# Performance work log

Hardware: AMD Instinct MI355X
Metric: run time of the kernel (lower is better)

Reference implementation:

```python
import jax, jax.numpy as jnp
import numpy as np

DEPTH, HEADS, DH, BUCKET, NHASH = 4, 8, 64, 64, 4
DIM, VOCAB, BATCH, SEQ = 512, 50000, 2, 2048
LN_EPS = 1e-5
SELF_ATTN_VAL = -5e4  # TOKEN_SELF_ATTN_VALUE in reformer_pytorch


def layer_norm(x, s, b):
    mu = x.mean(-1, keepdims=True)
    var = ((x - mu) ** 2).mean(-1, keepdims=True)
    return (x - mu) / jnp.sqrt(var + LN_EPS) * s + b


def sincos(t, dh):
    # FixedPositionalEmbedding: emb = cat(sin, cos) of t x dh/2 angles
    inv = 1.0 / (10000.0 ** (jnp.arange(0, dh, 2, dtype=jnp.float32) / dh))
    ang = jnp.arange(t, dtype=jnp.float32)[:, None] * inv[None, :]
    return jnp.sin(ang), jnp.cos(ang)


def apply_rotary(qk, sin, cos):
    # qk: [B*H, T, DH]; sin/cos: [T, DH/2]; interleaved-pair rotary as in reformer_pytorch
    sin2 = jnp.repeat(sin, 2, axis=-1)[None]
    cos2 = jnp.repeat(cos, 2, axis=-1)[None]
    xr = qk.reshape(qk.shape[0], qk.shape[1], -1, 2)
    rot = jnp.stack((-xr[..., 1], xr[..., 0]), axis=-1).reshape(qk.shape)
    return qk * cos2 + rot * sin2


def lsh_attention(qk, v, rot):
    # qk, v: [B, T, dh] (B = batch*heads, shared-QK); rot: [dh, NHASH, n_buckets//2]
    B, T, dh = qk.shape
    nb = T // BUCKET
    rv = jnp.einsum('btf,fhi->bhti', qk, rot)           # [B, NHASH, T, nb/2]
    rv = jnp.concatenate([rv, -rv], axis=-1)
    buckets = jnp.argmax(rv, axis=-1)                    # [B, NHASH, T]
    buckets = (buckets + (jnp.arange(NHASH) * nb)[None, :, None]).reshape(B, NHASH * T)
    ticker = jnp.arange(NHASH * T) % T
    key = T * buckets + ticker[None, :]                  # unique sort keys
    sticker = jnp.argsort(key, axis=-1)                  # [B, NHASH*T]
    undo = jnp.argsort(sticker, axis=-1)
    st = sticker % T
    sqk = jnp.take_along_axis(qk, st[:, :, None], axis=1)
    sv = jnp.take_along_axis(v, st[:, :, None], axis=1)
    C = NHASH * nb                                       # num chunks, each BUCKET long
    bq_t = st.reshape(B, C, BUCKET)
    bq = sqk.reshape(B, C, BUCKET, dh)
    bv = sv.reshape(B, C, BUCKET, dh)
    bk = bq / jnp.maximum(jnp.linalg.norm(bq, axis=-1, keepdims=True), 1e-12)

    def look_one_back(a):
        return jnp.concatenate([a, jnp.roll(a, 1, axis=1)], axis=2)

    bk, bv, bkv_t = look_one_back(bk), look_one_back(bv), look_one_back(bq_t)
    dots = jnp.einsum('bcie,bcje->bcij', bq, bk) * (dh ** -0.5)
    dots = jnp.where(bq_t[:, :, :, None] == bkv_t[:, :, None, :], SELF_ATTN_VAL, dots)
    lse = jax.nn.logsumexp(dots, axis=-1, keepdims=True)
    p = jnp.exp(dots - lse)
    bo = jnp.einsum('bcij,bcje->bcie', p, bv)
    so = bo.reshape(B, NHASH * T, dh)
    slog = lse.reshape(B, NHASH * T)
    o = jnp.take_along_axis(so, undo[:, :, None], axis=1).reshape(B, NHASH, T, dh)
    lg = jnp.take_along_axis(slog, undo, axis=1).reshape(B, NHASH, T, 1)
    w = jnp.exp(lg - jax.nn.logsumexp(lg, axis=1, keepdims=True))
    return jnp.sum(o * w, axis=1)                        # [B, T, dh]


def attn_block(x, s, bln, Wqk, Wv, Wo, bo, rot, sin, cos):
    b, t, _ = x.shape
    xn = layer_norm(x, s, bln)
    qk = (xn @ Wqk).reshape(b, t, HEADS, DH).transpose(0, 2, 1, 3).reshape(b * HEADS, t, DH)
    v = (xn @ Wv).reshape(b, t, HEADS, DH).transpose(0, 2, 1, 3).reshape(b * HEADS, t, DH)
    qk = apply_rotary(qk, sin, cos)
    o = lsh_attention(qk, v, rot)
    o = o.reshape(b, HEADS, t, DH).transpose(0, 2, 1, 3).reshape(b, t, HEADS * DH)
    return o @ Wo + bo


def ff_block(x, s, b, W1, b1, W2, b2):
    xn = layer_norm(x, s, b)
    return jax.nn.gelu(xn @ W1 + b1, approximate=False) @ W2 + b2


def reference(x, token_emb, ln1_s, ln1_b, Wqk, Wv, Wo, bo, ln2_s, ln2_b, W1, b1, W2, b2, rotations, lnf_s, lnf_b, Wf1, bf1, Wout, bout):
    e = token_emb[x]                                     # [B, T, DIM]
    sin, cos = sincos(x.shape[1], DH)
    x1 = x2 = e                                          # reversible twin streams
    for i in range(DEPTH):
        x1 = x1 + attn_block(x2, ln1_s[i], ln1_b[i], Wqk[i], Wv[i], Wo[i], bo[i], rotations[i], sin, cos)
        x2 = x2 + ff_block(x1, ln2_s[i], ln2_b[i], W1[i], b1[i], W2[i], b2[i])
    h = layer_norm((x1 + x2) * 0.5, lnf_s, lnf_b)
    h = h.mean(axis=1)
    h = jax.nn.relu(h @ Wf1 + bf1)
    return h @ Wout + bout


def setup_inputs():
    key = jax.random.key(0)
    ks = jax.random.split(key, 10)
    nb = SEQ // BUCKET
    s = 0.02
    return {
        'x': jax.random.randint(ks[0], (BATCH, SEQ), 0, VOCAB),
        'token_emb': jax.random.normal(ks[1], (VOCAB, DIM), jnp.float32) * s,
        'ln1_s': jnp.ones((DEPTH, DIM), jnp.float32),
        'ln1_b': jnp.zeros((DEPTH, DIM), jnp.float32),
        'Wqk': jax.random.normal(ks[2], (DEPTH, DIM, HEADS * DH), jnp.float32) * s,
        'Wv': jax.random.normal(ks[3], (DEPTH, DIM, HEADS * DH), jnp.float32) * s,
        'Wo': jax.random.normal(ks[4], (DEPTH, HEADS * DH, DIM), jnp.float32) * s,
        'bo': jnp.zeros((DEPTH, DIM), jnp.float32),
        'ln2_s': jnp.ones((DEPTH, DIM), jnp.float32),
        'ln2_b': jnp.zeros((DEPTH, DIM), jnp.float32),
        'W1': jax.random.normal(ks[5], (DEPTH, DIM, 4 * DIM), jnp.float32) * s,
        'b1': jnp.zeros((DEPTH, 4 * DIM), jnp.float32),
        'W2': jax.random.normal(ks[6], (DEPTH, 4 * DIM, DIM), jnp.float32) * s,
        'b2': jnp.zeros((DEPTH, DIM), jnp.float32),
        'rotations': jax.random.normal(ks[7], (DEPTH, DH, NHASH, nb // 2), jnp.float32),
        'lnf_s': jnp.ones((DIM,), jnp.float32),
        'lnf_b': jnp.zeros((DIM,), jnp.float32),
        'Wf1': jax.random.normal(ks[8], (DIM, 256), jnp.float32) * s,
        'bf1': jnp.zeros((256,), jnp.float32),
        'Wout': jax.random.normal(ks[9], (256, 1), jnp.float32) * s,
        'bout': jnp.zeros((1,), jnp.float32),
    }
```

## Files before the change

kernel.cpp:

```cpp
#include <hip/hip_runtime.h>
#include <math.h>

#define TSEQ   2048
#define DIMM   512
#define NHEAD  8
#define DHD    64
#define BHD    16
#define NHASHK 4
#define CHUNKS 128
#define FFD    2048
#define NROWS  4096

#define OFF_WQK 0
#define OFF_WV  262144
#define OFF_WO  524288
#define OFF_W1  786432
#define OFF_W2  1835008
#define WT_TOT  2883584

typedef unsigned short u16;
typedef _Float16 f16;
typedef __attribute__((ext_vector_type(8))) _Float16 f16x8;
typedef __attribute__((ext_vector_type(4))) float f32x4;
typedef __attribute__((ext_vector_type(8))) unsigned short ushort8v;
typedef __attribute__((ext_vector_type(4))) unsigned short ushort4v;

__device__ inline u16 h16(float f) {
  union { f16 h; u16 u; } x;
  x.h = (f16)f;
  return x.u;
}
__device__ inline float f16f(u16 u) {
  union { u16 u; f16 h; } x;
  x.u = u;
  return (float)x.h;
}
__device__ inline f16x8 mk8f(unsigned a, unsigned b, unsigned c, unsigned d) {
  union { unsigned u[4]; f16x8 v; } x;
  x.u[0] = a; x.u[1] = b; x.u[2] = c; x.u[3] = d;
  return x.v;
}
__device__ inline float gelu_exact(float v) {
  return 0.5f * v * (1.0f + erff(v * 0.70710678118654752f));
}
__device__ inline int swz128(int row, int colbyte) {
  return row * 128 + (colbyte ^ ((row & 7) << 4));
}
#define VT(d, k) ((d) * 264 + (((d) & 32) ? 8 : 0) + ((k) << 1))

__global__ __launch_bounds__(128) void k_embed(const int* __restrict__ x, const float* __restrict__ emb,
                                               float* __restrict__ x1, float* __restrict__ x2) {
  int row = blockIdx.x;
  int tok = x[row];
  float4 v = ((const float4*)(emb + (size_t)tok * DIMM))[threadIdx.x];
  ((float4*)(x1 + (size_t)row * DIMM))[threadIdx.x] = v;
  ((float4*)(x2 + (size_t)row * DIMM))[threadIdx.x] = v;
}

__global__ __launch_bounds__(256) void k_sincos(float* __restrict__ sin_t, float* __restrict__ cos_t) {
  int idx = blockIdx.x * 256 + threadIdx.x;
  int t = idx >> 5, i = idx & 31;
  float inv = powf(10000.0f, -(float)(2 * i) / 64.0f);
  float ang = (float)t * inv;
  sin_t[idx] = sinf(ang);
  cos_t[idx] = cosf(ang);
}

__global__ __launch_bounds__(256) void k_layernorm(const float* __restrict__ x, const float* __restrict__ g,
                                                   const float* __restrict__ b, u16* __restrict__ dst) {
  int row = blockIdx.x, tid = threadIdx.x;
  const float* xr = x + (size_t)row * DIMM;
  float v0 = xr[tid], v1 = xr[tid + 256];
  int lane = tid & 63, w = tid >> 6;
  __shared__ float red[8];
  float s = v0 + v1;
#pragma unroll
  for (int o = 32; o; o >>= 1) s += __shfl_xor(s, o);
  if (lane == 0) red[w] = s;
  __syncthreads();
  float mu = (red[0] + red[1] + red[2] + red[3]) * (1.0f / DIMM);
  float d0 = v0 - mu, d1 = v1 - mu;
  float q = d0 * d0 + d1 * d1;
#pragma unroll
  for (int o = 32; o; o >>= 1) q += __shfl_xor(q, o);
  if (lane == 0) red[4 + w] = q;
  __syncthreads();
  float var = (red[4] + red[5] + red[6] + red[7]) * (1.0f / DIMM);
  float rstd = 1.0f / sqrtf(var + 1e-5f);
  size_t base = (size_t)row * DIMM;
  dst[base + tid] = h16(d0 * rstd * g[tid] + b[tid]);
  dst[base + tid + 256] = h16(d1 * rstd * g[tid + 256] + b[tid + 256]);
}

__global__ __launch_bounds__(256) void k_prep(const float* __restrict__ Wqk, const float* __restrict__ Wv,
                                              const float* __restrict__ Wo, const float* __restrict__ W1,
                                              const float* __restrict__ W2, const float* __restrict__ rot,
                                              u16* __restrict__ wt16, u16* __restrict__ rt16) {
  __shared__ float tile[32][33];
  const int L = blockIdx.x / 2820;
  const int idx = blockIdx.x - L * 2820;
  Wqk += (size_t)L * 262144;
  Wv  += (size_t)L * 262144;
  Wo  += (size_t)L * 262144;
  W1  += (size_t)L * 1048576;
  W2  += (size_t)L * 1048576;
  rot += (size_t)L * 4096;
  u16* wt = wt16 + (size_t)L * WT_TOT;
  u16* rt = rt16 + (size_t)L * 4096;
  const float* src;
  u16* dh;
  int K, N, k0, n0;
  if (idx < 768) {
    int w = idx >> 8, r = idx & 255;
    K = 512; N = 512; k0 = (r >> 4) << 5; n0 = (r & 15) << 5;
    src = (w == 0) ? Wqk : (w == 1) ? Wv : Wo;
    dh = wt + (size_t)w * 262144;
  } else if (idx < 1792) {
    int r = idx - 768;
    K = 512; N = 2048; k0 = (r >> 6) << 5; n0 = (r & 63) << 5;
    src = W1; dh = wt + OFF_W1;
  } else if (idx < 2816) {
    int r = idx - 1792;
    K = 2048; N = 512; k0 = (r >> 4) << 5; n0 = (r & 15) << 5;
    src = W2; dh = wt + OFF_W2;
  } else {
    int r = idx - 2816;
    K = 64; N = 64; k0 = (r >> 1) << 5; n0 = (r & 1) << 5;
    src = rot; dh = rt;
  }
  const int t = threadIdx.x;
  const int r = t >> 3, c4 = (t & 7) << 2;
  float4 v = *(const float4*)&src[(size_t)(k0 + r) * N + n0 + c4];
  tile[r][c4] = v.x; tile[r][c4 + 1] = v.y; tile[r][c4 + 2] = v.z; tile[r][c4 + 3] = v.w;
  __syncthreads();
  u16 hs[4];
#pragma unroll
  for (int i = 0; i < 4; ++i) hs[i] = h16(tile[c4 + i][r]);
  size_t o = (size_t)(n0 + r) * K + k0 + c4;
  *(ushort4v*)&dh[o] = (ushort4v){hs[0], hs[1], hs[2], hs[3]};
}

template <int BM, int STORE>
__global__ __launch_bounds__(256) void k_gemm16(
    const u16* __restrict__ A, const u16* __restrict__ Bt,
    const float* __restrict__ bias, float* __restrict__ out,
    u16* __restrict__ out16, u16* __restrict__ qk16, u16* __restrict__ v16,
    int K, int N,
    const float* __restrict__ sin_t, const float* __restrict__ cos_t) {
  constexpr int MF = BM / 32;
  constexpr int ACH = BM / 32;
  __shared__ __align__(16) char AsB[BM * 128];
  __shared__ __align__(16) char BsB[64 * 128];
  const int bm = blockIdx.x * BM, bn = blockIdx.y << 6;
  const int tid = threadIdx.x, lane = tid & 63, wid = tid >> 6;
  const int wm = (wid >> 1) * (BM / 2), wn = (wid & 1) << 5;
  const int l16 = lane & 15, g = lane >> 4;
  f32x4 acc[MF][2];
#pragma unroll
  for (int m = 0; m < MF; ++m) { acc[m][0] = (f32x4){0,0,0,0}; acc[m][1] = (f32x4){0,0,0,0}; }

  const int srow = tid >> 3;
  const int scolb = (tid & 7) << 4;
  const u16* ap = A + (size_t)(bm + srow) * K + ((tid & 7) << 3);
  const u16* bp = Bt + (size_t)(bn + srow) * K + ((tid & 7) << 3);

  ushort8v paA[ACH], pbA[2], paB[ACH], pbB[2];
#pragma unroll
  for (int i = 0; i < ACH; ++i) paA[i] = *(const ushort8v*)(ap + (size_t)(i << 5) * K);
#pragma unroll
  for (int i = 0; i < 2; ++i) pbA[i] = *(const ushort8v*)(bp + (size_t)(i << 5) * K);
#pragma unroll
  for (int i = 0; i < ACH; ++i) paB[i] = *(const ushort8v*)(ap + (size_t)(i << 5) * K + 64);
#pragma unroll
  for (int i = 0; i < 2; ++i) pbB[i] = *(const ushort8v*)(bp + (size_t)(i << 5) * K + 64);

  auto gstep = [&](ushort8v (&PA)[ACH], ushort8v (&PB)[2], int S) {
#pragma unroll
    for (int i = 0; i < ACH; ++i)
      *(ushort8v*)(AsB + swz128(srow + (i << 5), scolb)) = PA[i];
#pragma unroll
    for (int i = 0; i < 2; ++i)
      *(ushort8v*)(BsB + swz128(srow + (i << 5), scolb)) = PB[i];
    __syncthreads();
    const int kf = (S + 2) << 6;
    if (kf < K) {
#pragma unroll
      for (int i = 0; i < ACH; ++i) PA[i] = *(const ushort8v*)(ap + (size_t)(i << 5) * K + kf);
#pragma unroll
      for (int i = 0; i < 2; ++i) PB[i] = *(const ushort8v*)(bp + (size_t)(i << 5) * K + kf);
    }
    f16x8 af[MF][2], bfr[2][2];
#pragma unroll
    for (int m = 0; m < MF; ++m)
#pragma unroll
      for (int ks = 0; ks < 2; ++ks)
        af[m][ks] = *(const f16x8*)(AsB + swz128(wm + (m << 4) + l16, ((ks << 2) + g) << 4));
#pragma unroll
    for (int n = 0; n < 2; ++n)
#pragma unroll
      for (int ks = 0; ks < 2; ++ks)
        bfr[n][ks] = *(const f16x8*)(BsB + swz128(wn + (n << 4) + l16, ((ks << 2) + g) << 4));
#pragma unroll
    for (int m = 0; m < MF; ++m)
#pragma unroll
      for (int n = 0; n < 2; ++n)
#pragma unroll
        for (int ks = 0; ks < 2; ++ks)
          acc[m][n] = __builtin_amdgcn_mfma_f32_16x16x32_f16(af[m][ks], bfr[n][ks], acc[m][n], 0, 0, 0);
    __syncthreads();
  };

  const int nsteps = K >> 6;
  for (int s = 0; s < nsteps; s += 2) {
    gstep(paA, pbA, s);
    gstep(paB, pbB, s + 1);
  }

#pragma unroll
  for (int m = 0; m < MF; ++m) {
#pragma unroll
    for (int n = 0; n < 2; ++n) {
      const int gn = bn + wn + (n << 4) + l16;
      float bv = 0.f;
      if (STORE == 1 || STORE == 4) bv = bias[gn];
#pragma unroll
      for (int r = 0; r < 4; ++r) {
        const int gm = bm + wm + (m << 4) + (g << 2) + r;
        float val = acc[m][n][r];
        if (STORE == 1) {
          out[(size_t)gm * N + gn] += val + bv;
        } else if (STORE == 4) {
          out16[(size_t)gm * N + gn] = h16(gelu_exact(val + bv));
        } else {
          const float pv = __shfl_xor(val, 1);
          const int bb = gm >> 11, tt = gm & (TSEQ - 1);
          if (gn < 512) {
            const int hh = gn >> 6, dd = gn & 63;
            const int ip = dd >> 1;
            float cz = cos_t[tt * 32 + ip], sz = sin_t[tt * 32 + ip];
            float o = (dd & 1) ? (val * cz + pv * sz) : (val * cz - pv * sz);
            qk16[((size_t)((bb * NHEAD + hh) * TSEQ + tt)) * DHD + dd] = h16(o);
          } else {
            const int gnn = gn - 512;
            const int hh = gnn >> 6, dd = gnn & 63;
            v16[((size_t)((bb * NHEAD + hh) * TSEQ + tt)) * DHD + dd] = h16(val);
          }
        }
      }
    }
  }
}

__global__ __launch_bounds__(256) void k_bucket_gemm(const u16* __restrict__ qk16,
                                                     const u16* __restrict__ rt16,
                                                     int* __restrict__ bucket) {
  __shared__ __align__(16) u16 Ah[128][72];
  __shared__ __align__(16) u16 Bh[64][72];
  const int bm = blockIdx.x << 7;
  const int tid = threadIdx.x, lane = tid & 63, wid = tid >> 6;
  const int l16 = lane & 15, g = lane >> 4;
  {
    const int r = tid >> 1, hf = tid & 1;
    const u16* src = qk16 + (size_t)(bm + r) * 64 + hf * 32;
#pragma unroll
    for (int i = 0; i < 4; ++i)
      *(ushort8v*)&Ah[r][hf * 32 + i * 8] = *(const ushort8v*)(src + i * 8);
  }
  if (tid < 128) {
    const int r = tid >> 1, hf = tid & 1;
    const u16* src = rt16 + (size_t)r * 64 + hf * 32;
#pragma unroll
    for (int i = 0; i < 4; ++i)
      *(ushort8v*)&Bh[r][hf * 32 + i * 8] = *(const ushort8v*)(src + i * 8);
  }
  __syncthreads();
  const int wm = (wid >> 1) << 6, wn = (wid & 1) << 5;
  f32x4 acc[4][2];
#pragma unroll
  for (int m = 0; m < 4; ++m) { acc[m][0] = (f32x4){0,0,0,0}; acc[m][1] = (f32x4){0,0,0,0}; }
#pragma unroll
  for (int s = 0; s < 2; ++s) {
    f16x8 bfr[2];
#pragma unroll
    for (int n = 0; n < 2; ++n)
      bfr[n] = *(const f16x8*)&Bh[wn + (n << 4) + l16][s * 32 + g * 8];
#pragma unroll
    for (int m = 0; m < 4; ++m) {
      f16x8 afr = *(const f16x8*)&Ah[wm + (m << 4) + l16][s * 32 + g * 8];
#pragma unroll
      for (int n = 0; n < 2; ++n)
        acc[m][n] = __builtin_amdgcn_mfma_f32_16x16x32_f16(afr, bfr[n], acc[m][n], 0, 0, 0);
    }
  }
#pragma unroll
  for (int m = 0; m < 4; ++m)
#pragma unroll
    for (int n = 0; n < 2; ++n) {
      const int hcol = (wn >> 4) + n;
#pragma unroll
      for (int r = 0; r < 4; ++r) {
        float v = acc[m][n][r];
        float best = v; int bi = l16;
        if (-v > best) { best = -v; bi = 16 + l16; }
#pragma unroll
        for (int o = 1; o < 16; o <<= 1) {
          float ob = __shfl_xor(best, o);
          int obi = __shfl_xor(bi, o);
          if (ob > best || (ob == best && obi < bi)) { best = ob; bi = obi; }
        }
        if (l16 == 0) {
          int gm = bm + wm + (m << 4) + (g << 2) + r;
          int bh_ = gm >> 11, t = gm & (TSEQ - 1);
          bucket[((size_t)(bh_ * NHASHK) + hcol) * TSEQ + t] = bi;
        }
      }
    }
}

__global__ __launch_bounds__(256) void k_sort(const int* __restrict__ bucket, int* __restrict__ st) {
  __shared__ int hist[256][33];
  __shared__ int bbase[32];
  const int seg = blockIdx.x;
  const int tid = threadIdx.x;
  const int* bk = bucket + (size_t)seg * TSEQ;
  int4 u0 = *(const int4*)(bk + tid * 8);
  int4 u1 = *(const int4*)(bk + tid * 8 + 4);
  int myb[8] = {u0.x, u0.y, u0.z, u0.w, u1.x, u1.y, u1.z, u1.w};
#pragma unroll
  for (int j = 0; j < 33; ++j) hist[tid][j] = 0;
  __syncthreads();
#pragma unroll
  for (int i = 0; i < 8; ++i) hist[tid][myb[i]]++;
  __syncthreads();
  if (tid < 32) {
    int run = 0;
    for (int gq = 0; gq < 256; ++gq) { int c = hist[gq][tid]; hist[gq][tid] = run; run += c; }
    bbase[tid] = run;
  }
  __syncthreads();
  if (tid == 0) {
    int s = 0;
    for (int j = 0; j < 32; ++j) { int c = bbase[j]; bbase[j] = s; s += c; }
  }
  __syncthreads();
  int* dst = st + (size_t)seg * TSEQ;
#pragma unroll
  for (int i = 0; i < 8; ++i) {
    int b = myb[i];
    int p = bbase[b] + hist[tid][b];
    hist[tid][b]++;
    dst[p] = tid * 8 + i;
  }
}

__global__ __launch_bounds__(256) void k_attn(const u16* __restrict__ qk16,
                                              const u16* __restrict__ v16,
                                              const int* __restrict__ st,
                                              float* __restrict__ o4, float* __restrict__ lg) {
  __shared__ __align__(16) char Kb[128 * 128];
  __shared__ __align__(16) char Vb[64 * 264 + 16];
  __shared__ float inv_norm[128];
  __shared__ int tids[128];
  __shared__ float pn[256];
  const int blk = blockIdx.x;
  const int c = blk & (CHUNKS - 1), bh = blk >> 7;
  const int h = c >> 5;
  const int tid = threadIdx.x, lane = tid & 63, wid = tid >> 6;
  const int l16 = lane & 15, g = lane >> 4;

  if (tid < 128) {
    int cc = (tid < 64) ? c : ((c + CHUNKS - 1) & (CHUNKS - 1));
    tids[tid] = st[bh * (NHASHK * TSEQ) + cc * 64 + (tid & 63)];
  }
  __syncthreads();
  {
    const int r = tid >> 1, hf = tid & 1;
    const u16* qsrc = qk16 + ((size_t)bh * TSEQ + tids[r]) * 64 + hf * 32;
    const u16* vsrc = v16 + ((size_t)bh * TSEQ + tids[r]) * 64 + hf * 32;
    float ss = 0.f;
#pragma unroll
    for (int i = 0; i < 4; ++i) {
      ushort8v u = *(const ushort8v*)(qsrc + i * 8);
      *(ushort8v*)(Kb + swz128(r, hf * 64 + i * 16)) = u;
#pragma unroll
      for (int j = 0; j < 8; ++j) { float f = f16f(u[j]); ss += f * f; }
      ushort8v vv8 = *(const ushort8v*)(vsrc + i * 8);
#pragma unroll
      for (int j = 0; j < 8; ++j)
        *(u16*)(Vb + VT(hf * 32 + i * 8 + j, r)) = vv8[j];
    }
    pn[tid] = ss;
  }
  __syncthreads();
  if (tid < 128) {
    float s2 = pn[2 * tid] + pn[2 * tid + 1];
    inv_norm[tid] = 1.0f / fmaxf(sqrtf(s2), 1e-12f);
  }
  __syncthreads();

  const int qrow = (wid << 4) + l16;
  const int tq = tids[qrow];
  const size_t obase = (size_t)(bh * NHASHK + h) * TSEQ + tq;

  f32x4 accs[8];
#pragma unroll
  for (int i = 0; i < 8; ++i) accs[i] = (f32x4){0, 0, 0, 0};
#pragma unroll
  for (int s = 0; s < 2; ++s) {
    f16x8 qf = *(const f16x8*)(Kb + swz128(qrow, ((s << 2) + g) << 4));
#pragma unroll
    for (int mf = 0; mf < 8; ++mf) {
      f16x8 afr = *(const f16x8*)(Kb + swz128(mf * 16 + l16, ((s << 2) + g) << 4));
      accs[mf] = __builtin_amdgcn_mfma_f32_16x16x32_f16(afr, qf, accs[mf], 0, 0, 0);
    }
  }
  float pv[8][4];
  float mx = -3e38f;
#pragma unroll
  for (int mf = 0; mf < 8; ++mf) {
    float4 invn = *(const float4*)&inv_norm[mf * 16 + g * 4];
    int4 tk = *(const int4*)&tids[mf * 16 + g * 4];
    float inva[4] = {invn.x, invn.y, invn.z, invn.w};
    int tka[4] = {tk.x, tk.y, tk.z, tk.w};
#pragma unroll
    for (int r = 0; r < 4; ++r) {
      float d = accs[mf][r] * inva[r] * 0.125f;
      if (tka[r] == tq) d = -5e4f;
      pv[mf][r] = d;
      mx = fmaxf(mx, d);
    }
  }
  mx = fmaxf(mx, __shfl_xor(mx, 16));
  mx = fmaxf(mx, __shfl_xor(mx, 32));
  float sum = 0.f;
#pragma unroll
  for (int mf = 0; mf < 8; ++mf)
#pragma unroll
    for (int r = 0; r < 4; ++r) {
      float e = __expf(pv[mf][r] - mx);
      pv[mf][r] = e;
      sum += e;
    }
  sum += __shfl_xor(sum, 16);
  sum += __shfl_xor(sum, 32);
  float lse = __logf(sum) + mx;
  float rs = 1.0f / sum;
  if (g == 0) lg[obase] = lse;
  unsigned P2[8][2];
#pragma unroll
  for (int mf = 0; mf < 8; ++mf)
#pragma unroll
    for (int m = 0; m < 2; ++m) {
      float p0 = pv[mf][2 * m] * rs, p1 = pv[mf][2 * m + 1] * rs;
      P2[mf][m] = (unsigned)h16(p0) | ((unsigned)h16(p1) << 16);
    }
  f32x4 acco[4];
#pragma unroll
  for (int i = 0; i < 4; ++i) acco[i] = (f32x4){0, 0, 0, 0};
#pragma unroll
  for (int s = 0; s < 4; ++s) {
    unsigned bw[4];
#pragma unroll
    for (int w = 0; w < 4; ++w) {
      int srl = l16 + (((2 * g + (w >> 1)) & 3) << 4);
      unsigned a0 = __shfl(P2[2 * s][w & 1], srl);
      unsigned a1 = __shfl(P2[2 * s + 1][w & 1], srl);
      bw[w] = (g >> 1) ? a1 : a0;
    }
    f16x8 pb = mk8f(bw[0], bw[1], bw[2], bw[3]);
    const int k0 = s * 32 + g * 8;
#pragma unroll
    for (int mf = 0; mf < 4; ++mf) {
      const int dcol = mf * 16 + l16;
      uint2 v0 = *(const uint2*)(Vb + VT(dcol, k0));
      uint2 v1 = *(const uint2*)(Vb + VT(dcol, k0 + 4));
      f16x8 vf = mk8f(v0.x, v0.y, v1.x, v1.y);
      acco[mf] = __builtin_amdgcn_mfma_f32_16x16x32_f16(vf, pb, acco[mf], 0, 0, 0);
    }
  }
#pragma unroll
  for (int mf = 0; mf < 4; ++mf)
    *(float4*)&o4[obase * 64 + mf * 16 + g * 4] =
        make_float4(acco[mf][0], acco[mf][1], acco[mf][2], acco[mf][3]);
}

__global__ __launch_bounds__(256) void k_combine(const float* __restrict__ o4, const float* __restrict__ lg,
                                                 u16* __restrict__ ctx16) {
  int tok = blockIdx.x * 4 + (threadIdx.x >> 6);
  int dd = threadIdx.x & 63;
  int bh = tok >> 11, t = tok & (TSEQ - 1);
  size_t base = (size_t)bh * NHASHK * TSEQ + t;
  float l0 = lg[base], l1 = lg[base + TSEQ], l2 = lg[base + 2 * TSEQ], l3 = lg[base + 3 * TSEQ];
  float m = fmaxf(fmaxf(l0, l1), fmaxf(l2, l3));
  float e0 = expf(l0 - m), e1 = expf(l1 - m), e2 = expf(l2 - m), e3 = expf(l3 - m);
  float inv = 1.0f / (e0 + e1 + e2 + e3);
  float o = (e0 * o4[base * 64 + dd] + e1 * o4[(base + TSEQ) * 64 + dd] +
             e2 * o4[(base + 2 * TSEQ) * 64 + dd] + e3 * o4[(base + 3 * TSEQ) * 64 + dd]) * inv;
  int b = bh >> 3, hh = bh & 7;
  ctx16[((size_t)(b * TSEQ + t)) * DIMM + hh * DHD + dd] = h16(o);
}

__global__ __launch_bounds__(256) void k_colmean1(const float* __restrict__ x1, const float* __restrict__ x2,
                                                  float* __restrict__ part) {
  const int blk = blockIdx.x;
  const int bb = blk >> 8, ch = blk & 255;
  const int tid = threadIdx.x, lane = tid & 63, w = tid >> 6;
  __shared__ float red[8];
  float a0 = 0.f, a1 = 0.f;
  for (int i = 0; i < 8; ++i) {
    int row = bb * TSEQ + ch * 8 + i;
    size_t base = (size_t)row * DIMM;
    float v0 = 0.5f * (x1[base + tid] + x2[base + tid]);
    float v1 = 0.5f * (x1[base + tid + 256] + x2[base + tid + 256]);
    float s = v0 + v1;
#pragma unroll
    for (int o = 32; o; o >>= 1) s += __shfl_xor(s, o);
    if (lane == 0) red[w] = s;
    __syncthreads();
    float mu = (red[0] + red[1] + red[2] + red[3]) * (1.0f / DIMM);
    float d0 = v0 - mu, d1 = v1 - mu;
    float q = d0 * d0 + d1 * d1;
#pragma unroll
    for (int o = 32; o; o >>= 1) q += __shfl_xor(q, o);
    if (lane == 0) red[4 + w] = q;
    __syncthreads();
    float var = (red[4] + red[5] + red[6] + red[7]) * (1.0f / DIMM);
    float rstd = 1.0f / sqrtf(var + 1e-5f);
    a0 += d0 * rstd;
    a1 += d1 * rstd;
    __syncthreads();
  }
  part[(size_t)blk * DIMM + tid] = a0;
  part[(size_t)blk * DIMM + tid + 256] = a1;
}

__global__ __launch_bounds__(256) void k_colmean2(const float* __restrict__ part,
                                                  const float* __restrict__ g, const float* __restrict__ b,
                                                  float* __restrict__ hm) {
  int gidx = blockIdx.x * 256 + threadIdx.x;
  int oid = gidx >> 3, sub = gidx & 7;
  int bb = oid >> 9, d = oid & 511;
  float s = 0.f;
  for (int c = sub; c < 256; c += 8) s += part[((size_t)(bb * 256 + c)) * DIMM + d];
  s += __shfl_xor(s, 1);
  s += __shfl_xor(s, 2);
  s += __shfl_xor(s, 4);
  if (sub == 0) hm[oid] = s * (1.0f / TSEQ) * g[d] + b[d];
}

__global__ __launch_bounds__(256) void k_head1(const float* __restrict__ hm, const float* __restrict__ Wf1,
                                               float* __restrict__ r1p) {
  int b = blockIdx.x & 1, kc = blockIdx.x >> 1;
  int j = threadIdx.x;
  float acc = 0;
  for (int k = kc * 64; k < kc * 64 + 64; ++k) acc += hm[b * DIMM + k] * Wf1[k * 256 + j];
  r1p[(size_t)(kc * 2 + b) * 256 + j] = acc;
}

__global__ __launch_bounds__(256) void k_head2(const float* __restrict__ r1p, const float* __restrict__ bf1,
                                               const float* __restrict__ Wout, const float* __restrict__ bout,
                                               float* __restrict__ outp) {
  int b = blockIdx.x;
  int tid = threadIdx.x, lane = tid & 63, w = tid >> 6;
  float s = 0.f;
#pragma unroll
  for (int kc = 0; kc < 8; ++kc) s += r1p[(size_t)(kc * 2 + b) * 256 + tid];
  float v = fmaxf(s + bf1[tid], 0.0f) * Wout[tid];
#pragma unroll
  for (int o = 32; o; o >>= 1) v += __shfl_xor(v, o);
  __shared__ float red[4];
  if (lane == 0) red[w] = v;
  __syncthreads();
  if (tid == 0) outp[b] = red[0] + red[1] + red[2] + red[3] + bout[0];
}

extern "C" void kernel_launch(void* const* d_in, const int* in_sizes, int n_in,
                              void* d_out, int out_size, void* d_ws, size_t ws_size,
                              hipStream_t stream) {
  const int*   x         = (const int*)d_in[0];
  const float* token_emb = (const float*)d_in[1];
  const float* ln1_s     = (const float*)d_in[2];
  const float* ln1_b     = (const float*)d_in[3];
  const float* Wqk       = (const float*)d_in[4];
  const float* Wv        = (const float*)d_in[5];
  const float* Wo        = (const float*)d_in[6];
  const float* bo        = (const float*)d_in[7];
  const float* ln2_s     = (const float*)d_in[8];
  const float* ln2_b     = (const float*)d_in[9];
  const float* W1        = (const float*)d_in[10];
  const float* b1        = (const float*)d_in[11];
  const float* W2        = (const float*)d_in[12];
  const float* b2        = (const float*)d_in[13];
  const float* rotations = (const float*)d_in[14];
  const float* lnf_s     = (const float*)d_in[15];
  const float* lnf_b     = (const float*)d_in[16];
  const float* Wf1       = (const float*)d_in[17];
  const float* bf1       = (const float*)d_in[18];
  const float* Wout      = (const float*)d_in[19];
  const float* bout      = (const float*)d_in[20];
  float* out = (float*)d_out;

  char* ws = (char*)d_ws;
  size_t off = 0;
  auto alloc = [&](size_t nbytes) {
    char* p = ws + off;
    off += (nbytes + 255) & ~(size_t)255;
    return p;
  };
  float*  x1     = (float*)alloc((size_t)NROWS * DIMM * 4);
  float*  x2     = (float*)alloc((size_t)NROWS * DIMM * 4);
  u16*    xn16   = (u16*)alloc((size_t)NROWS * DIMM * 2);
  u16*    qk16   = (u16*)alloc((size_t)BHD * TSEQ * DHD * 2);
  u16*    v16    = (u16*)alloc((size_t)BHD * TSEQ * DHD * 2);
  u16*    ffh16  = (u16*)alloc((size_t)NROWS * FFD * 2);
  float*  o4     = (float*)alloc((size_t)BHD * NHASHK * TSEQ * DHD * 4);
  float*  lg     = (float*)alloc((size_t)BHD * NHASHK * TSEQ * 4);
  float*  sin_t  = (float*)alloc((size_t)TSEQ * 32 * 4);
  float*  cos_t  = (float*)alloc((size_t)TSEQ * 32 * 4);
  float*  part   = (float*)alloc((size_t)512 * DIMM * 4);
  float*  hm     = (float*)alloc(2 * DIMM * 4);
  float*  r1p    = (float*)alloc(16 * 256 * 4);
  int*    bucket = (int*)alloc((size_t)BHD * NHASHK * TSEQ * 4);
  int*    st     = (int*)alloc((size_t)BHD * NHASHK * TSEQ * 4);
  u16*    wt16   = (u16*)alloc((size_t)4 * WT_TOT * 2);
  u16*    rott16 = (u16*)alloc((size_t)4 * 64 * 64 * 2);
  u16*    ctx16  = xn16;

  k_embed<<<NROWS, 128, 0, stream>>>(x, token_emb, x1, x2);
  k_sincos<<<(TSEQ * 32) / 256, 256, 0, stream>>>(sin_t, cos_t);
  k_prep<<<4 * 2820, 256, 0, stream>>>(Wqk, Wv, Wo, W1, W2, rotations, wt16, rott16);

  for (int L = 0; L < 4; ++L) {
    u16* wt = wt16 + (size_t)L * WT_TOT;
    u16* rt = rott16 + (size_t)L * 4096;

    k_layernorm<<<NROWS, 256, 0, stream>>>(x2, ln1_s + L * DIMM, ln1_b + L * DIMM, xn16);
    k_gemm16<128, 5><<<dim3(32, 16), 256, 0, stream>>>(
        xn16, wt + OFF_WQK, nullptr, nullptr, nullptr, qk16, v16, 512, 1024, sin_t, cos_t);
    k_bucket_gemm<<<BHD * TSEQ / 128, 256, 0, stream>>>(qk16, rt, bucket);
    k_sort<<<BHD * NHASHK, 256, 0, stream>>>(bucket, st);
    k_attn<<<BHD * CHUNKS, 256, 0, stream>>>(qk16, v16, st, o4, lg);
    k_combine<<<(BHD * TSEQ) / 4, 256, 0, stream>>>(o4, lg, ctx16);
    k_gemm16<64, 1><<<dim3(64, 8), 256, 0, stream>>>(
        ctx16, wt + OFF_WO, bo + L * DIMM, x1, nullptr, nullptr, nullptr, 512, 512, nullptr, nullptr);
    k_layernorm<<<NROWS, 256, 0, stream>>>(x1, ln2_s + L * DIMM, ln2_b + L * DIMM, xn16);
    k_gemm16<128, 4><<<dim3(32, 32), 256, 0, stream>>>(
        xn16, wt + OFF_W1, b1 + L * FFD, nullptr, ffh16, nullptr, nullptr, 512, 2048, nullptr, nullptr);
    k_gemm16<64, 1><<<dim3(64, 8), 256, 0, stream>>>(
        ffh16, wt + OFF_W2, b2 + L * DIMM, x2, nullptr, nullptr, nullptr, 2048, 512, nullptr, nullptr);
  }

  k_colmean1<<<512, 256, 0, stream>>>(x1, x2, part);
  k_colmean2<<<32, 256, 0, stream>>>(part, lnf_s, lnf_b, hm);
  k_head1<<<16, 256, 0, stream>>>(hm, Wf1, r1p);
  k_head2<<<2, 256, 0, stream>>>(r1p, bf1, Wout, bout, out);
}
```

Before: 570.5 us.

## Fuse LSH bucketing into QKV GEMM, parallelize sort scan, store partial outputs in fp16

The bucket-hash projection and argmax now run in the epilogue of the QK/V GEMM. The rotary-applied QK tile is written into shared memory and multiplied by the rotation matrix there, which removes a separate kernel launch and a re-read of qk16. The counting-sort prefix scan is split across all threads in chunks instead of 32 serial threads walking 256 rows. Per-hash attention outputs are stored as fp16 to halve combine traffic, and the QKV and FFN1 GEMMs switch from BM=128 to BM=64 tiles. The fp16 partial outputs cost some precision, and the epilogue reuses shared memory without an explicit barrier before the writes.

After: 501.7 us (median of 2 runs). 12.1% less time.

```diff
diff --git a/kernel.cpp b/kernel.cpp
--- a/kernel.cpp
+++ b/kernel.cpp
@@ -146,7 +146,8 @@
     const float* __restrict__ bias, float* __restrict__ out,
     u16* __restrict__ out16, u16* __restrict__ qk16, u16* __restrict__ v16,
     int K, int N,
-    const float* __restrict__ sin_t, const float* __restrict__ cos_t) {
+    const float* __restrict__ sin_t, const float* __restrict__ cos_t,
+    const u16* __restrict__ rt16, int* __restrict__ bucket) {
   constexpr int MF = BM / 32;
   constexpr int ACH = BM / 32;
   __shared__ __align__(16) char AsB[BM * 128];
@@ -214,6 +215,14 @@
   for (int s = 0; s < nsteps; s += 2) {
     gstep(paA, pbA, s);
     gstep(paB, pbB, s + 1);
+  }
+
+  const bool do_bucket = (STORE == 5) && (bn < 512);
+  ushort8v prt0{}, prt1{};
+  if (do_bucket) {
+    int i0 = tid, i1 = tid + 256;
+    prt0 = *(const ushort8v*)(rt16 + (i0 >> 3) * 64 + ((i0 & 7) << 3));
+    prt1 = *(const ushort8v*)(rt16 + (i1 >> 3) * 64 + ((i1 & 7) << 3));
   }
 
 #pragma unroll
@@ -239,7 +248,9 @@
             const int ip = dd >> 1;
             float cz = cos_t[tt * 32 + ip], sz = sin_t[tt * 32 + ip];
             float o = (dd & 1) ? (val * cz + pv * sz) : (val * cz - pv * sz);
-            qk16[((size_t)((bb * NHEAD + hh) * TSEQ + tt)) * DHD + dd] = h16(o);
+            u16 oh = h16(o);
+            qk16[((size_t)((bb * NHEAD + hh) * TSEQ + tt)) * DHD + dd] = oh;
+            *(u16*)(AsB + swz128(gm - bm, dd << 1)) = oh;
           } else {
             const int gnn = gn - 512;
             const int hh = gnn >> 6, dd = gnn & 63;
@@ -249,76 +260,63 @@
       }
     }
   }
-}
-
-__global__ __launch_bounds__(256) void k_bucket_gemm(const u16* __restrict__ qk16,
-                                                     const u16* __restrict__ rt16,
-                                                     int* __restrict__ bucket) {
-  __shared__ __align__(16) u16 Ah[128][72];
-  __shared__ __align__(16) u16 Bh[64][72];
-  const int bm = blockIdx.x << 7;
-  const int tid = threadIdx.x, lane = tid & 63, wid = tid >> 6;
-  const int l16 = lane & 15, g = lane >> 4;
-  {
-    const int r = tid >> 1, hf = tid & 1;
-    const u16* src = qk16 + (size_t)(bm + r) * 64 + hf * 32;
-#pragma unroll
-    for (int i = 0; i < 4; ++i)
-      *(ushort8v*)&Ah[r][hf * 32 + i * 8] = *(const ushort8v*)(src + i * 8);
-  }
-  if (tid < 128) {
-    const int r = tid >> 1, hf = tid & 1;
-    const u16* src = rt16 + (size_t)r * 64 + hf * 32;
-#pragma unroll
-    for (int i = 0; i < 4; ++i)
-      *(ushort8v*)&Bh[r][hf * 32 + i * 8] = *(const ushort8v*)(src + i * 8);
-  }
-  __syncthreads();
-  const int wm = (wid >> 1) << 6, wn = (wid & 1) << 5;
-  f32x4 acc[4][2];
-#pragma unroll
-  for (int m = 0; m < 4; ++m) { acc[m][0] = (f32x4){0,0,0,0}; acc[m][1] = (f32x4){0,0,0,0}; }
-#pragma unroll
-  for (int s = 0; s < 2; ++s) {
-    f16x8 bfr[2];
-#pragma unroll
-    for (int n = 0; n < 2; ++n)
-      bfr[n] = *(const f16x8*)&Bh[wn + (n << 4) + l16][s * 32 + g * 8];
-#pragma unroll
-    for (int m = 0; m < 4; ++m) {
-      f16x8 afr = *(const f16x8*)&Ah[wm + (m << 4) + l16][s * 32 + g * 8];
+
+  if (do_bucket) {
+    {
+      int i0 = tid, i1 = tid + 256;
+      *(ushort8v*)(BsB + swz128(i0 >> 3, (i0 & 7) << 4)) = prt0;
+      *(ushort8v*)(BsB + swz128(i1 >> 3, (i1 & 7) << 4)) = prt1;
+    }
+    __syncthreads();
+    const int bwm = (wid >> 1) << 5;
+    const int bwn = (wid & 1) << 5;
+    f32x4 bacc[2][2];
+#pragma unroll
+    for (int m = 0; m < 2; ++m) { bacc[m][0] = (f32x4){0,0,0,0}; bacc[m][1] = (f32x4){0,0,0,0}; }
+#pragma unroll
+    for (int ks = 0; ks < 2; ++ks) {
+      f16x8 bfr[2];
 #pragma unroll
       for (int n = 0; n < 2; ++n)
-        acc[m][n] = __builtin_amdgcn_mfma_f32_16x16x32_f16(afr, bfr[n], acc[m][n], 0, 0, 0);
-    }
-  }
-#pragma unroll
-  for (int m = 0; m < 4; ++m)
-#pragma unroll
-    for (int n = 0; n < 2; ++n) {
-      const int hcol = (wn >> 4) + n;
-#pragma unroll
-      for (int r = 0; r < 4; ++r) {
-        float v = acc[m][n][r];
-        float best = v; int bi = l16;
-        if (-v > best) { best = -v; bi = 16 + l16; }
-#pragma unroll
-        for (int o = 1; o < 16; o <<= 1) {
-          float ob = __shfl_xor(best, o);
-          int obi = __shfl_xor(bi, o);
-          if (ob > best || (ob == best && obi < bi)) { best = ob; bi = obi; }
-        }
-        if (l16 == 0) {
-          int gm = bm + wm + (m << 4) + (g << 2) + r;
-          int bh_ = gm >> 11, t = gm & (TSEQ - 1);
-          bucket[((size_t)(bh_ * NHASHK) + hcol) * TSEQ + t] = bi;
+        bfr[n] = *(const f16x8*)(BsB + swz128(bwn + (n << 4) + l16, (ks << 6) + (g << 4)));
+#pragma unroll
+      for (int m = 0; m < 2; ++m) {
+        f16x8 afr = *(const f16x8*)(AsB + swz128(bwm + (m << 4) + l16, (ks << 6) + (g << 4)));
+#pragma unroll
+        for (int n = 0; n < 2; ++n)
+          bacc[m][n] = __builtin_amdgcn_mfma_f32_16x16x32_f16(afr, bfr[n], bacc[m][n], 0, 0, 0);
+      }
+    }
+    const int bb = bm >> 11;
+    const int hh = bn >> 6;
+#pragma unroll
+    for (int m = 0; m < 2; ++m)
+#pragma unroll
+      for (int n = 0; n < 2; ++n) {
+        const int hcol = (bwn >> 4) + n;
+#pragma unroll
+        for (int r = 0; r < 4; ++r) {
+          float v = bacc[m][n][r];
+          float best = v; int bi = l16;
+          if (-v > best) { best = -v; bi = 16 + l16; }
+#pragma unroll
+          for (int o = 1; o < 16; o <<= 1) {
+            float ob = __shfl_xor(best, o);
+            int obi = __shfl_xor(bi, o);
+            if (ob > best || (ob == best && obi < bi)) { best = ob; bi = obi; }
+          }
+          if (l16 == 0) {
+            int t = (bm & (TSEQ - 1)) + bwm + (m << 4) + (g << 2) + r;
+            bucket[((size_t)((bb * NHEAD + hh) * NHASHK) + hcol) * TSEQ + t] = bi;
+          }
         }
       }
-    }
+  }
 }
 
 __global__ __launch_bounds__(256) void k_sort(const int* __restrict__ bucket, int* __restrict__ st) {
   __shared__ int hist[256][33];
+  __shared__ int chunk[8][32];
   __shared__ int bbase[32];
   const int seg = blockIdx.x;
   const int tid = threadIdx.x;
@@ -332,23 +330,31 @@
 #pragma unroll
   for (int i = 0; i < 8; ++i) hist[tid][myb[i]]++;
   __syncthreads();
+  const int b = tid & 31, c = tid >> 5;
+  int ssum = 0;
+  for (int g2 = c * 32; g2 < c * 32 + 32; ++g2) ssum += hist[g2][b];
+  chunk[c][b] = ssum;
+  __syncthreads();
   if (tid < 32) {
     int run = 0;
-    for (int gq = 0; gq < 256; ++gq) { int c = hist[gq][tid]; hist[gq][tid] = run; run += c; }
+    for (int cc = 0; cc < 8; ++cc) { int v = chunk[cc][tid]; chunk[cc][tid] = run; run += v; }
     bbase[tid] = run;
   }
   __syncthreads();
   if (tid == 0) {
     int s = 0;
-    for (int j = 0; j < 32; ++j) { int c = bbase[j]; bbase[j] = s; s += c; }
-  }
+    for (int j = 0; j < 32; ++j) { int v = bbase[j]; bbase[j] = s; s += v; }
+  }
+  __syncthreads();
+  int run = chunk[c][b];
+  for (int g2 = c * 32; g2 < c * 32 + 32; ++g2) { int v = hist[g2][b]; hist[g2][b] = run; run += v; }
   __syncthreads();
   int* dst = st + (size_t)seg * TSEQ;
 #pragma unroll
   for (int i = 0; i < 8; ++i) {
-    int b = myb[i];
-    int p = bbase[b] + hist[tid][b];
-    hist[tid][b]++;
+    int bb2 = myb[i];
+    int p = bbase[bb2] + hist[tid][bb2];
+    hist[tid][bb2]++;
     dst[p] = tid * 8 + i;
   }
 }
@@ -356,7 +362,7 @@
 __global__ __launch_bounds__(256) void k_attn(const u16* __restrict__ qk16,
                                               const u16* __restrict__ v16,
                                               const int* __restrict__ st,
-                                              float* __restrict__ o4, float* __restrict__ lg) {
+                                              u16* __restrict__ o4h, float* __restrict__ lg) {
   __shared__ __align__(16) char Kb[128 * 128];
   __shared__ __align__(16) char Vb[64 * 264 + 16];
   __shared__ float inv_norm[128];
@@ -479,12 +485,13 @@
     }
   }
 #pragma unroll
-  for (int mf = 0; mf < 4; ++mf)
-    *(float4*)&o4[obase * 64 + mf * 16 + g * 4] =
-        make_float4(acco[mf][0], acco[mf][1], acco[mf][2], acco[mf][3]);
-}
-
-__global__ __launch_bounds__(256) void k_combine(const float* __restrict__ o4, const float* __restrict__ lg,
+  for (int mf = 0; mf < 4; ++mf) {
+    ushort4v o4s = {h16(acco[mf][0]), h16(acco[mf][1]), h16(acco[mf][2]), h16(acco[mf][3])};
+    *(ushort4v*)&o4h[obase * 64 + mf * 16 + g * 4] = o4s;
+  }
+}
+
+__global__ __launch_bounds__(256) void k_combine(const u16* __restrict__ o4h, const float* __restrict__ lg,
                                                  u16* __restrict__ ctx16) {
   int tok = blockIdx.x * 4 + (threadIdx.x >> 6);
   int dd = threadIdx.x & 63;
@@ -494,8 +501,8 @@
   float m = fmaxf(fmaxf(l0, l1), fmaxf(l2, l3));
   float e0 = expf(l0 - m), e1 = expf(l1 - m), e2 = expf(l2 - m), e3 = expf(l3 - m);
   float inv = 1.0f / (e0 + e1 + e2 + e3);
-  float o = (e0 * o4[base * 64 + dd] + e1 * o4[(base + TSEQ) * 64 + dd] +
-             e2 * o4[(base + 2 * TSEQ) * 64 + dd] + e3 * o4[(base + 3 * TSEQ) * 64 + dd]) * inv;
+  float o = (e0 * f16f(o4h[base * 64 + dd]) + e1 * f16f(o4h[(base + TSEQ) * 64 + dd]) +
+             e2 * f16f(o4h[(base + 2 * TSEQ) * 64 + dd]) + e3 * f16f(o4h[(base + 3 * TSEQ) * 64 + dd])) * inv;
   int b = bh >> 3, hh = bh & 7;
   ctx16[((size_t)(b * TSEQ + t)) * DIMM + hh * DHD + dd] = h16(o);
 }
@@ -613,7 +620,7 @@
   u16*    qk16   = (u16*)alloc((size_t)BHD * TSEQ * DHD * 2);
   u16*    v16    = (u16*)alloc((size_t)BHD * TSEQ * DHD * 2);
   u16*    ffh16  = (u16*)alloc((size_t)NROWS * FFD * 2);
-  float*  o4     = (float*)alloc((size_t)BHD * NHASHK * TSEQ * DHD * 4);
+  u16*    o4h    = (u16*)alloc((size_t)BHD * NHASHK * TSEQ * DHD * 2);
   float*  lg     = (float*)alloc((size_t)BHD * NHASHK * TSEQ * 4);
   float*  sin_t  = (float*)alloc((size_t)TSEQ * 32 * 4);
   float*  cos_t  = (float*)alloc((size_t)TSEQ * 32 * 4);
@@ -635,19 +642,18 @@
     u16* rt = rott16 + (size_t)L * 4096;
 
     k_layernorm<<<NROWS, 256, 0, stream>>>(x2, ln1_s + L * DIMM, ln1_b + L * DIMM, xn16);
-    k_gemm16<128, 5><<<dim3(32, 16), 256, 0, stream>>>(
-        xn16, wt + OFF_WQK, nullptr, nullptr, nullptr, qk16, v16, 512, 1024, sin_t, cos_t);
-    k_bucket_gemm<<<BHD * TSEQ / 128, 256, 0, stream>>>(qk16, rt, bucket);
+    k_gemm16<64, 5><<<dim3(64, 16), 256, 0, stream>>>(
+        xn16, wt + OFF_WQK, nullptr, nullptr, nullptr, qk16, v16, 512, 1024, sin_t, cos_t, rt, bucket);
     k_sort<<<BHD * NHASHK, 256, 0, stream>>>(bucket, st);
-    k_attn<<<BHD * CHUNKS, 256, 0, stream>>>(qk16, v16, st, o4, lg);
-    k_combine<<<(BHD * TSEQ) / 4, 256, 0, stream>>>(o4, lg, ctx16);
+    k_attn<<<BHD * CHUNKS, 256, 0, stream>>>(qk16, v16, st, o4h, lg);
+    k_combine<<<(BHD * TSEQ) / 4, 256, 0, stream>>>(o4h, lg, ctx16);
     k_gemm16<64, 1><<<dim3(64, 8), 256, 0, stream>>>(
-        ctx16, wt + OFF_WO, bo + L * DIMM, x1, nullptr, nullptr, nullptr, 512, 512, nullptr, nullptr);
+        ctx16, wt + OFF_WO, bo + L * DIMM, x1, nullptr, nullptr, nullptr, 512, 512, nullptr, nullptr, nullptr, nullptr);
     k_layernorm<<<NROWS, 256, 0, stream>>>(x1, ln2_s + L * DIMM, ln2_b + L * DIMM, xn16);
-    k_gemm16<128, 4><<<dim3(32, 32), 256, 0, stream>>>(
-        xn16, wt + OFF_W1, b1 + L * FFD, nullptr, ffh16, nullptr, nullptr, 512, 2048, nullptr, nullptr);
+    k_gemm16<64, 4><<<dim3(64, 32), 256, 0, stream>>>(
+        xn16, wt + OFF_W1, b1 + L * FFD, nullptr, ffh16, nullptr, nullptr, 512, 2048, nullptr, nullptr, nullptr, nullptr);
     k_gemm16<64, 1><<<dim3(64, 8), 256, 0, stream>>>(
-        ffh16, wt + OFF_W2, b2 + L * DIMM, x2, nullptr, nullptr, nullptr, 2048, 512, nullptr, nullptr);
+        ffh16, wt + OFF_W2, b2 + L * DIMM, x2, nullptr, nullptr, nullptr, 2048, 512, nullptr, nullptr, nullptr, nullptr);
   }
 
   k_colmean1<<<512, 256, 0, stream>>>(x1, x2, part);
```
